# Optimization experiments

Hardware: AMD Instinct MI355X
Metric: run time of the kernel (lower is better)

The kernel has to match this reference:

```python
import jax, jax.numpy as jnp
import numpy as np

# Dims chosen per init_kwargs / input_specs
B, CIN, H, W = 16, 384, 64, 64
HEADS, HD = 4, 24
D = HEADS * HD                 # 96, per-pixel feature dim after head split
NMOD = 2                       # PartitionalClustering (hard), FuzzyClustering (soft)
NSTREAM = 1 + 2 * NMOD         # p + (k,v) per clustering module = 5
AG = 8                         # agents_hw = (8,8) -> 64 agent tokens
CL = 2                         # clusters_hw = (2,2) -> 4 clusters per module
M_PER = CL * CL
M_ALL = NMOD * M_PER           # 8 total clusters (sim_alpha/sim_beta size)


def setup_inputs() -> dict:
    key = jax.random.key(0)
    ks = jax.random.split(key, 4)
    x = jax.random.normal(ks[0], (B, CIN, H, W), jnp.float32)
    # proj: 1x1 pointwise linear CIN -> NSTREAM*D
    W1 = jax.random.normal(ks[1], (CIN, NSTREAM * D), jnp.float32) * 0.02
    b1 = jnp.zeros((NSTREAM * D,), jnp.float32)
    # proj2: 1x1 pointwise linear D -> CIN
    W2 = jax.random.normal(ks[2], (D, CIN), jnp.float32) * 0.02
    b2 = jnp.zeros((CIN,), jnp.float32)
    sim_alpha = jnp.ones((M_ALL,), jnp.float32)
    sim_beta = jnp.zeros((M_ALL,), jnp.float32)
    return {"x": x, "W1": W1, "b1": b1, "W2": W2, "b2": b2,
            "sim_alpha": sim_alpha, "sim_beta": sim_beta}


def _pool(t, oh, ow):
    # exact adaptive avg pool when h%oh==0 and w%ow==0
    b, c, h, w = t.shape
    return t.reshape(b, c, oh, h // oh, ow, w // ow).mean(axis=(3, 5))


def _cluster_agg(k, kc, v, vc, hard):
    # k: (b,c,N)  kc: (b,m,c)  v: (b,N,c)  vc: (b,m,c)
    # similarity = negative squared euclidean distance (use_cosine=False)
    d2 = (kc ** 2).sum(-1)[..., None] + (k ** 2).sum(1)[:, None, :] \
         - 2.0 * jnp.einsum('bmc,bcn->bmn', kc, k)          # (b,m,N)
    sim = -d2
    if hard:   # PartitionalClustering: hard one-hot assignment over clusters
        w = jax.nn.one_hot(jnp.argmax(sim, axis=1), sim.shape[1], axis=1, dtype=k.dtype)
    else:      # FuzzyClustering: soft assignment over clusters
        w = jax.nn.softmax(sim, axis=1)
    agg = vc + jnp.einsum('bmn,bnc->bmc', w, v)
    return agg / (1.0 + w.sum(-1, keepdims=True))            # cluster-bias normalization


def _cosine(a, p):
    # a: (b,M,c), p: (b,c,N) -> cosine similarity (b,M,N)
    an = a / (jnp.linalg.norm(a, axis=-1, keepdims=True) + 1e-6)
    pn = p / (jnp.linalg.norm(p, axis=1, keepdims=True) + 1e-6)
    return jnp.einsum('bmc,bcn->bmn', an, pn)


def reference(x, W1, b1, W2, b2, sim_alpha, sim_beta):
    # proj (1x1): (B,CIN,H,W) -> (B, NSTREAM*D, H, W)
    y = jnp.einsum('bchw,cd->bdhw', x, W1) + b1[None, :, None, None]
    b = B * HEADS
    y = y.reshape(B, NSTREAM, D, H, W).transpose(1, 0, 2, 3, 4)
    y = y.reshape(NSTREAM, b, HD, H, W)
    p = y[0]                                   # (b, HD, H, W)
    r = y[1:].reshape(NMOD, 2, b, HD, H, W)    # (module, k/v, b, HD, H, W)

    aggs = []
    for i in range(NMOD):
        k, v = r[i, 0], r[i, 1]
        kc = _pool(k, CL, CL).reshape(b, HD, M_PER).transpose(0, 2, 1)  # (b,m,c)
        vc = _pool(v, CL, CL).reshape(b, HD, M_PER).transpose(0, 2, 1)
        ka = _pool(k, AG, AG).reshape(b, HD, AG * AG)                   # (b,c,N)
        va = _pool(v, AG, AG).reshape(b, HD, AG * AG).transpose(0, 2, 1)
        aggs.append(_cluster_agg(ka, kc, va, vc, hard=(i == 0)))
    agg = jnp.concatenate(aggs, axis=1)        # (b, M_ALL, HD)

    pa = _pool(p, AG, AG).reshape(b, HD, AG * AG)                       # (b,c,N)
    sim = sim_alpha[None, :, None] * _cosine(agg, pa) + sim_beta[None, :, None]
    assign = jax.nn.softmax(sim, axis=1)        # over clusters
    out = jnp.einsum('bmc,bmn->bcn', agg, assign).reshape(b, HD, AG, AG)
    out = jax.image.resize(out, (b, HD, H, W), method='bilinear')
    out = out.reshape(B, D, H, W)
    # proj2 (1x1): D -> CIN
    return jnp.einsum('bchw,co->bohw', out, W2) + b2[None, :, None, None]
```

## Files before the change

### kernel.cpp

```cpp
#include <hip/hip_runtime.h>
#include <math.h>

#define NB     16
#define NCIN   384
#define NHD    24
#define NDIM   96
#define NSTR   5
#define NDT    480

__global__ void __launch_bounds__(256) k_pool(const float* __restrict__ x,
                                              float* __restrict__ x8) {
    __shared__ float part[64][17];
    const int plane = blockIdx.x;
    const int t = threadIdx.x;
    const float4* xp = reinterpret_cast<const float4*>(x + (size_t)plane * 4096);
    const int chunk = t & 15;
    const int rloc  = t >> 4;
#pragma unroll
    for (int rr = 0; rr < 4; ++rr) {
        int row = rr * 16 + rloc;
        float4 v = xp[rr * 256 + t];
        part[row][chunk] = v.x + v.y + v.z + v.w;
    }
    __syncthreads();
    if (t < 64) {
        int py = t >> 3, px = t & 7;
        float s = 0.f;
#pragma unroll
        for (int r = 0; r < 8; ++r)
            s += part[py * 8 + r][px * 2] + part[py * 8 + r][px * 2 + 1];
        x8[(size_t)plane * 64 + t] = s * (1.f / 64.f);
    }
}

#define KC 64
__global__ void __launch_bounds__(256) k_proj(const float* __restrict__ x8,
                                              const float* __restrict__ W1,
                                              const float* __restrict__ b1,
                                              float* __restrict__ y8) {
    __shared__ float AL[KC][32];
    __shared__ float BL[KC][64];
    const int b    = blockIdx.y >> 1;
    const int pix0 = (blockIdx.y & 1) * 32;
    const int d0   = blockIdx.x * 64;
    const int tid  = threadIdx.x;
    const int pxg  = (tid & 15) * 2;
    const int dg   = (tid >> 4) * 4;
    float acc[2][4] = {};
    for (int c0 = 0; c0 < 384; c0 += KC) {
        __syncthreads();
#pragma unroll
        for (int i = 0; i < 2; ++i) {
            int f = tid + i * 256;
            int c = f >> 3, pg = f & 7;
            *reinterpret_cast<float4*>(&AL[c][pg * 4]) =
                *reinterpret_cast<const float4*>(&x8[(b * 384 + c0 + c) * 64 + pix0 + pg * 4]);
        }
#pragma unroll
        for (int i = 0; i < 4; ++i) {
            int f = tid + i * 256;
            int c = f >> 4, jg = f & 15;
            int d = d0 + jg * 4;
            float4 v = make_float4(0.f, 0.f, 0.f, 0.f);
            if (d < NDT) v = *reinterpret_cast<const float4*>(&W1[(c0 + c) * NDT + d]);
            *reinterpret_cast<float4*>(&BL[c][jg * 4]) = v;
        }
        __syncthreads();
#pragma unroll 8
        for (int c = 0; c < KC; ++c) {
            float2 a = *reinterpret_cast<const float2*>(&AL[c][pxg]);
            float4 w = *reinterpret_cast<const float4*>(&BL[c][dg]);
            acc[0][0] += a.x * w.x; acc[0][1] += a.x * w.y;
            acc[0][2] += a.x * w.z; acc[0][3] += a.x * w.w;
            acc[1][0] += a.y * w.x; acc[1][1] += a.y * w.y;
            acc[1][2] += a.y * w.z; acc[1][3] += a.y * w.w;
        }
    }
    if (d0 + dg < NDT) {
        float4 bv = *reinterpret_cast<const float4*>(&b1[d0 + dg]);
#pragma unroll
        for (int p = 0; p < 2; ++p) {
            int pix = pix0 + pxg + p;
            float4 v = make_float4(acc[p][0] + bv.x, acc[p][1] + bv.y,
                                   acc[p][2] + bv.z, acc[p][3] + bv.w);
            *reinterpret_cast<float4*>(&y8[(size_t)(b * 64 + pix) * NDT + d0 + dg]) = v;
        }
    }
}

__global__ void __launch_bounds__(256) k_cluster(const float* __restrict__ y8,
                                                 const float* __restrict__ salpha,
                                                 const float* __restrict__ sbeta,
                                                 float* __restrict__ out8) {
    __shared__ float sl[5][64][25];
    __shared__ float y2s[5][4][24];
    __shared__ float wb[2][64][5];
    __shared__ float aggL[8][25];
    __shared__ float anL[8][24];
    __shared__ float normL[8];

    const int bp = blockIdx.x;
    const int Bi = bp >> 2, h = bp & 3;
    const int tid = threadIdx.x;
    const int lane = tid & 63, wid = tid >> 6;

    for (int idx = tid; idx < 5 * 64 * 6; idx += 256) {
        int q = idx % 6;
        int row = idx / 6;
        int pix = row & 63, s = row >> 6;
        float4 v = *reinterpret_cast<const float4*>(
            &y8[(size_t)(Bi * 64 + pix) * NDT + s * NDIM + h * NHD + q * 4]);
        int c = q * 4;
        sl[s][pix][c]     = v.x;
        sl[s][pix][c + 1] = v.y;
        sl[s][pix][c + 2] = v.z;
        sl[s][pix][c + 3] = v.w;
    }
    __syncthreads();
    for (int idx = tid; idx < 5 * 4 * 24; idx += 256) {
        int c = idx % 24;
        int m = (idx / 24) & 3;
        int s = idx / 96;
        int my = m >> 1, mx = m & 1;
        float acc = 0.f;
#pragma unroll
        for (int ry = 0; ry < 4; ++ry)
#pragma unroll
            for (int rx = 0; rx < 4; ++rx)
                acc += sl[s][(my * 4 + ry) * 8 + mx * 4 + rx][c];
        y2s[s][m][c] = acc * (1.f / 16.f);
    }
    __syncthreads();
    if (wid < 2) {
        const int i = wid, ks = 1 + 2 * i;
        float ka[24];
        float sumk2 = 0.f;
#pragma unroll
        for (int c = 0; c < 24; ++c) { ka[c] = sl[ks][lane][c]; sumk2 += ka[c] * ka[c]; }
        float sim[4];
#pragma unroll
        for (int m = 0; m < 4; ++m) {
            float kc2 = 0.f, dt = 0.f;
#pragma unroll
            for (int c = 0; c < 24; ++c) {
                float kv = y2s[ks][m][c];
                kc2 += kv * kv; dt += kv * ka[c];
            }
            sim[m] = 2.f * dt - kc2 - sumk2;
        }
        float w[4];
        if (i == 0) {
            int am = 0; float bv = sim[0];
#pragma unroll
            for (int m = 1; m < 4; ++m) if (sim[m] > bv) { bv = sim[m]; am = m; }
#pragma unroll
            for (int m = 0; m < 4; ++m) w[m] = (m == am) ? 1.f : 0.f;
        } else {
            float mx = fmaxf(fmaxf(sim[0], sim[1]), fmaxf(sim[2], sim[3]));
            float sum = 0.f;
#pragma unroll
            for (int m = 0; m < 4; ++m) { w[m] = expf(sim[m] - mx); sum += w[m]; }
            float inv = 1.f / sum;
#pragma unroll
            for (int m = 0; m < 4; ++m) w[m] *= inv;
        }
#pragma unroll
        for (int m = 0; m < 4; ++m) wb[i][lane][m] = w[m];
    }
    __syncthreads();
    if (tid < 200) {
        int i = tid / 100, rem = tid % 100;
        int m = rem / 25, c = rem % 25;
        int vs = 2 + 2 * i;
        float s = 0.f;
#pragma unroll 8
        for (int n = 0; n < 64; ++n) {
            float wv = wb[i][n][m];
            s += (c < 24) ? wv * sl[vs][n][c] : wv;
        }
        aggL[i * 4 + m][c] = s;
    }
    __syncthreads();
    if (tid < 192) {
        int mm = tid / 24, c = tid % 24;
        int i = mm >> 2, m = mm & 3;
        aggL[mm][c] = (y2s[2 + 2 * i][m][c] + aggL[mm][c]) / (1.f + aggL[mm][24]);
    }
    __syncthreads();
    if (tid < 8) {
        float s = 0.f;
#pragma unroll
        for (int c = 0; c < 24; ++c) s += aggL[tid][c] * aggL[tid][c];
        normL[tid] = sqrtf(s) + 1e-6f;
    }
    __syncthreads();
    if (tid < 192) {
        int mm = tid / 24, c = tid % 24;
        anL[mm][c] = aggL[mm][c] / normL[mm];
    }
    __syncthreads();
    {
        const int n = lane;
        float pa[24]; float p2 = 0.f;
#pragma unroll
        for (int c = 0; c < 24; ++c) { pa[c] = sl[0][n][c]; p2 += pa[c] * pa[c]; }
        float pinv = 1.f / (sqrtf(p2) + 1e-6f);
        float s2[8];
#pragma unroll
        for (int mm = 0; mm < 8; ++mm) {
            float dt = 0.f;
#pragma unroll
            for (int c = 0; c < 24; ++c) dt += anL[mm][c] * pa[c];
            s2[mm] = salpha[mm] * (dt * pinv) + sbeta[mm];
        }
        float mx = s2[0];
#pragma unroll
        for (int mm = 1; mm < 8; ++mm) mx = fmaxf(mx, s2[mm]);
        float sum = 0.f;
#pragma unroll
        for (int mm = 0; mm < 8; ++mm) { s2[mm] = expf(s2[mm] - mx); sum += s2[mm]; }
        float inv = 1.f / sum;
        const int c0 = wid * 6;
#pragma unroll
        for (int cc = 0; cc < 6; ++cc) {
            int c = c0 + cc;
            float v = 0.f;
#pragma unroll
            for (int mm = 0; mm < 8; ++mm) v += aggL[mm][c] * (s2[mm] * inv);
            out8[(size_t)(Bi * NDIM + h * NHD + c) * 64 + n] = v;
        }
    }
}

__global__ void __launch_bounds__(256) k_proj2up(const float* __restrict__ out8,
                                                 const float* __restrict__ W2,
                                                 const float* __restrict__ b2,
                                                 float* __restrict__ out) {
    __shared__ float AL[96][64];
    __shared__ float WL[96][24];
    __shared__ float ZT[24][65];
    const int Bi = blockIdx.y;
    const int o0 = blockIdx.x * 24;
    const int tid = threadIdx.x;

#pragma unroll
    for (int i = 0; i < 6; ++i) {
        int f = tid + i * 256;
        int d = f >> 4, ng = f & 15;
        *reinterpret_cast<float4*>(&AL[d][ng * 4]) =
            *reinterpret_cast<const float4*>(&out8[(size_t)(Bi * NDIM + d) * 64 + ng * 4]);
    }
    for (int idx = tid; idx < 96 * 6; idx += 256) {
        int d = idx / 6, q = idx % 6;
        *reinterpret_cast<float4*>(&WL[d][q * 4]) =
            *reinterpret_cast<const float4*>(&W2[d * NCIN + o0 + q * 4]);
    }
    __syncthreads();
    {
        const int n = tid & 63, og = tid >> 6;
        float a0 = 0.f, a1 = 0.f, a2 = 0.f, a3 = 0.f, a4 = 0.f, a5 = 0.f;
#pragma unroll 8
        for (int d = 0; d < 96; ++d) {
            float a = AL[d][n];
            float2 w01 = *reinterpret_cast<const float2*>(&WL[d][og * 6 + 0]);
            float2 w23 = *reinterpret_cast<const float2*>(&WL[d][og * 6 + 2]);
            float2 w45 = *reinterpret_cast<const float2*>(&WL[d][og * 6 + 4]);
            a0 += a * w01.x; a1 += a * w01.y;
            a2 += a * w23.x; a3 += a * w23.y;
            a4 += a * w45.x; a5 += a * w45.y;
        }
        ZT[og * 6 + 0][n] = a0;
        ZT[og * 6 + 1][n] = a1;
        ZT[og * 6 + 2][n] = a2;
        ZT[og * 6 + 3][n] = a3;
        ZT[og * 6 + 4][n] = a4;
        ZT[og * 6 + 5][n] = a5;
    }
    __syncthreads();
#pragma unroll
    for (int pass = 0; pass < 2; ++pass) {
        int slot = pass * 256 + tid;
        if (slot < 24 * 16) {
            const int ol = slot >> 4, xq = slot & 15;
            const float bias = b2[o0 + ol];

            float uxb = 0.125f * (float)(xq * 4) - 0.4375f;
            float uxbc = fminf(fmaxf(uxb, 0.f), 7.f);
            const int ixb = (int)uxbc;
            float wa[4], wbx[4], wc[4];
#pragma unroll
            for (int j = 0; j < 4; ++j) {
                float ux  = 0.125f * (float)(xq * 4 + j) - 0.4375f;
                float uxc = fminf(fmaxf(ux, 0.f), 7.f);
                int ix0 = (int)uxc;
                int ix1 = ix0 + 1 > 7 ? 7 : ix0 + 1;
                float fx = uxc - (float)ix0;
                int k0 = ix0 - ixb, k1 = ix1 - ixb;
                wa[j]  = ((k0 == 0) ? (1.f - fx) : 0.f) + ((k1 == 0) ? fx : 0.f);
                wbx[j] = ((k0 == 1) ? (1.f - fx) : 0.f) + ((k1 == 1) ? fx : 0.f);
                wc[j]  = ((k1 == 2) ? fx : 0.f);
            }
            float zc0[8], zc1[8], zc2[8];
            {
                const int i1 = ixb + 1 > 7 ? 7 : ixb + 1;
                const int i2 = ixb + 2 > 7 ? 7 : ixb + 2;
#pragma unroll
                for (int iy = 0; iy < 8; ++iy) {
                    zc0[iy] = ZT[ol][iy * 8 + ixb];
                    zc1[iy] = ZT[ol][iy * 8 + i1];
                    zc2[iy] = ZT[ol][iy * 8 + i2];
                }
            }
            float* obase = out + (size_t)(Bi * NCIN + o0 + ol) * 4096 + xq * 4;
#pragma unroll
            for (int y = 0; y < 64; ++y) {
                const float u  = 0.125f * (float)y - 0.4375f;
                const float uc = fminf(fmaxf(u, 0.f), 7.f);
                const int iy0 = (int)uc;
                const int iy1 = iy0 + 1 > 7 ? 7 : iy0 + 1;
                const float fy = uc - (float)iy0;
                const float r0 = zc0[iy0] + fy * (zc0[iy1] - zc0[iy0]);
                const float r1 = zc1[iy0] + fy * (zc1[iy1] - zc1[iy0]);
                const float r2 = zc2[iy0] + fy * (zc2[iy1] - zc2[iy0]);
                float4 v;
                v.x = bias + wa[0] * r0 + wbx[0] * r1 + wc[0] * r2;
                v.y = bias + wa[1] * r0 + wbx[1] * r1 + wc[1] * r2;
                v.z = bias + wa[2] * r0 + wbx[2] * r1 + wc[2] * r2;
                v.w = bias + wa[3] * r0 + wbx[3] * r1 + wc[3] * r2;
                *reinterpret_cast<float4*>(obase + y * 64) = v;
            }
        }
    }
}

extern "C" void kernel_launch(void* const* d_in, const int* in_sizes, int n_in,
                              void* d_out, int out_size, void* d_ws, size_t ws_size,
                              hipStream_t stream) {
    const float* x  = (const float*)d_in[0];
    const float* W1 = (const float*)d_in[1];
    const float* b1 = (const float*)d_in[2];
    const float* W2 = (const float*)d_in[3];
    const float* b2 = (const float*)d_in[4];
    const float* sa = (const float*)d_in[5];
    const float* sb = (const float*)d_in[6];
    float* out = (float*)d_out;

    float* x8 = (float*)d_ws;
    float* y8 = x8 + 16 * 384 * 64;
    float* o8 = y8 + 1024 * 480;

    k_pool<<<dim3(16 * 384), dim3(256), 0, stream>>>(x, x8);
    k_proj<<<dim3(8, 32), dim3(256), 0, stream>>>(x8, W1, b1, y8);
    k_cluster<<<dim3(64), dim3(256), 0, stream>>>(y8, sa, sb, o8);
    k_proj2up<<<dim3(16, 16), dim3(256), 0, stream>>>(o8, W2, b2, out);
}
```

Measured before the change: 68.30 us.

## Fuse pool, projection, clustering and upsample into one cooperative kernel

Replaces the four separate kernel launches with a single cooperative kernel of 256 blocks, 16 per batch image. Stages are separated by per-batch atomic counter barriers in global memory, and shared memory is reused across stages through one flat buffer. The aim is to remove launch gaps between stages. In exchange, the pooling stage loses most of its parallelism: each block now walks 24 planes one after another with a block sync per plane, instead of spreading the work over thousands of blocks. Most blocks also sit idle during the clustering stage.

```diff
diff --git a/kernel.cpp b/kernel.cpp
--- a/kernel.cpp
+++ b/kernel.cpp
@@ -8,328 +8,359 @@
 #define NSTR   5
 #define NDT    480
 
-__global__ void __launch_bounds__(256) k_pool(const float* __restrict__ x,
-                                              float* __restrict__ x8) {
-    __shared__ float part[64][17];
-    const int plane = blockIdx.x;
-    const int t = threadIdx.x;
-    const float4* xp = reinterpret_cast<const float4*>(x + (size_t)plane * 4096);
-    const int chunk = t & 15;
-    const int rloc  = t >> 4;
-#pragma unroll
-    for (int rr = 0; rr < 4; ++rr) {
-        int row = rr * 16 + rloc;
-        float4 v = xp[rr * 256 + t];
-        part[row][chunk] = v.x + v.y + v.z + v.w;
-    }
+
+__device__ __forceinline__ void group_barrier(int* c, int target) {
+    __threadfence();
     __syncthreads();
-    if (t < 64) {
-        int py = t >> 3, px = t & 7;
-        float s = 0.f;
-#pragma unroll
-        for (int r = 0; r < 8; ++r)
-            s += part[py * 8 + r][px * 2] + part[py * 8 + r][px * 2 + 1];
-        x8[(size_t)plane * 64 + t] = s * (1.f / 64.f);
-    }
+    if (threadIdx.x == 0) {
+        __hip_atomic_fetch_add(c, 1, __ATOMIC_RELEASE, __HIP_MEMORY_SCOPE_AGENT);
+        while (__hip_atomic_load(c, __ATOMIC_ACQUIRE, __HIP_MEMORY_SCOPE_AGENT) < target)
+            __builtin_amdgcn_s_sleep(2);
+    }
+    __syncthreads();
+    __threadfence();
 }
 
-#define KC 64
-__global__ void __launch_bounds__(256) k_proj(const float* __restrict__ x8,
-                                              const float* __restrict__ W1,
-                                              const float* __restrict__ b1,
-                                              float* __restrict__ y8) {
-    __shared__ float AL[KC][32];
-    __shared__ float BL[KC][64];
-    const int b    = blockIdx.y >> 1;
-    const int pix0 = (blockIdx.y & 1) * 32;
-    const int d0   = blockIdx.x * 64;
-    const int tid  = threadIdx.x;
-    const int pxg  = (tid & 15) * 2;
-    const int dg   = (tid >> 4) * 4;
-    float acc[2][4] = {};
-    for (int c0 = 0; c0 < 384; c0 += KC) {
-        __syncthreads();
-#pragma unroll
-        for (int i = 0; i < 2; ++i) {
+__global__ void __launch_bounds__(256) k_fused(const float* __restrict__ x,
+                                               const float* __restrict__ W1,
+                                               const float* __restrict__ b1,
+                                               const float* __restrict__ W2,
+                                               const float* __restrict__ b2,
+                                               const float* __restrict__ salpha,
+                                               const float* __restrict__ sbeta,
+                                               float* __restrict__ out,
+                                               float* __restrict__ x8,
+                                               float* __restrict__ y8,
+                                               float* __restrict__ o8,
+                                               int* __restrict__ flags) {
+    __shared__ __align__(16) float smem[10100];
+    const int g   = blockIdx.x;
+    const int b   = g >> 4;
+    const int sub = g & 15;
+    const int tid = threadIdx.x;
+    int* cnt = flags + b * 3;
+
+    {
+        #define PART(r,cc) smem[(r)*17+(cc)]
+        const int chunk = tid & 15;
+        const int rloc  = tid >> 4;
+        for (int i = 0; i < 24; ++i) {
+            const int c = sub * 24 + i;
+            const float4* xp = reinterpret_cast<const float4*>(x + ((size_t)(b * 384 + c)) * 4096);
+#pragma unroll
+            for (int rr = 0; rr < 4; ++rr) {
+                int row = rr * 16 + rloc;
+                float4 v = xp[rr * 256 + tid];
+                PART(row, chunk) = v.x + v.y + v.z + v.w;
+            }
+            __syncthreads();
+            if (tid < 64) {
+                int py = tid >> 3, px = tid & 7;
+                float s = 0.f;
+#pragma unroll
+                for (int r = 0; r < 8; ++r)
+                    s += PART(py * 8 + r, px * 2) + PART(py * 8 + r, px * 2 + 1);
+                x8[(size_t)(b * 384 + c) * 64 + tid] = s * (1.f / 64.f);
+            }
+            __syncthreads();
+        }
+        #undef PART
+    }
+    group_barrier(cnt + 0, 16);
+
+    {
+        #define PAL(c,p) smem[(c)*32+(p)]
+        #define PBL(c,d) smem[2048+(c)*64+(d)]
+        const int pix0 = (sub >> 3) * 32;
+        const int d0   = (sub & 7) * 64;
+        const int pxg  = (tid & 15) * 2;
+        const int dg   = (tid >> 4) * 4;
+        float acc[2][4] = {};
+        for (int c0 = 0; c0 < 384; c0 += 64) {
+            __syncthreads();
+#pragma unroll
+            for (int i = 0; i < 2; ++i) {
+                int f = tid + i * 256;
+                int c = f >> 3, pg = f & 7;
+                *reinterpret_cast<float4*>(&PAL(c, pg * 4)) =
+                    *reinterpret_cast<const float4*>(&x8[(size_t)(b * 384 + c0 + c) * 64 + pix0 + pg * 4]);
+            }
+#pragma unroll
+            for (int i = 0; i < 4; ++i) {
+                int f = tid + i * 256;
+                int c = f >> 4, jg = f & 15;
+                int d = d0 + jg * 4;
+                float4 v = make_float4(0.f, 0.f, 0.f, 0.f);
+                if (d < NDT) v = *reinterpret_cast<const float4*>(&W1[(c0 + c) * NDT + d]);
+                *reinterpret_cast<float4*>(&PBL(c, jg * 4)) = v;
+            }
+            __syncthreads();
+#pragma unroll 8
+            for (int c = 0; c < 64; ++c) {
+                float2 a = *reinterpret_cast<const float2*>(&PAL(c, pxg));
+                float4 w = *reinterpret_cast<const float4*>(&PBL(c, dg));
+                acc[0][0] += a.x * w.x; acc[0][1] += a.x * w.y;
+                acc[0][2] += a.x * w.z; acc[0][3] += a.x * w.w;
+                acc[1][0] += a.y * w.x; acc[1][1] += a.y * w.y;
+                acc[1][2] += a.y * w.z; acc[1][3] += a.y * w.w;
+            }
+        }
+        if (d0 + dg < NDT) {
+            float4 bv = *reinterpret_cast<const float4*>(&b1[d0 + dg]);
+#pragma unroll
+            for (int p = 0; p < 2; ++p) {
+                int pix = pix0 + pxg + p;
+                float4 v = make_float4(acc[p][0] + bv.x, acc[p][1] + bv.y,
+                                       acc[p][2] + bv.z, acc[p][3] + bv.w);
+                *reinterpret_cast<float4*>(&y8[(size_t)(b * 64 + pix) * NDT + d0 + dg]) = v;
+            }
+        }
+        #undef PAL
+        #undef PBL
+    }
+    group_barrier(cnt + 1, 16);
+
+    if (sub < 4) {
+        #define SL(s,p,c)  smem[(s)*1600+(p)*25+(c)]
+        #define Y2S(s,m,c) smem[8000+((s)*4+(m))*24+(c)]
+        #define WBM(i,n,m) smem[8480+((i)*64+(n))*5+(m)]
+        #define AGG(mm,c)  smem[9120+(mm)*25+(c)]
+        #define ANL(mm,c)  smem[9320+(mm)*24+(c)]
+        #define NRM(mm)    smem[9512+(mm)]
+        const int Bi = b, h = sub;
+        const int lane = tid & 63, wid = tid >> 6;
+
+        for (int idx = tid; idx < 5 * 64 * 6; idx += 256) {
+            int q = idx % 6;
+            int row = idx / 6;
+            int pix = row & 63, s = row >> 6;
+            float4 v = *reinterpret_cast<const float4*>(
+                &y8[(size_t)(Bi * 64 + pix) * NDT + s * NDIM + h * NHD + q * 4]);
+            int c = q * 4;
+            SL(s, pix, c)     = v.x;
+            SL(s, pix, c + 1) = v.y;
+            SL(s, pix, c + 2) = v.z;
+            SL(s, pix, c + 3) = v.w;
+        }
+        __syncthreads();
+        for (int idx = tid; idx < 5 * 4 * 24; idx += 256) {
+            int c = idx % 24;
+            int m = (idx / 24) & 3;
+            int s = idx / 96;
+            int my = m >> 1, mx = m & 1;
+            float acc = 0.f;
+#pragma unroll
+            for (int ry = 0; ry < 4; ++ry)
+#pragma unroll
+                for (int rx = 0; rx < 4; ++rx)
+                    acc += SL(s, (my * 4 + ry) * 8 + mx * 4 + rx, c);
+            Y2S(s, m, c) = acc * (1.f / 16.f);
+        }
+        __syncthreads();
+        if (wid < 2) {
+            const int i = wid, ks = 1 + 2 * i;
+            float ka[24];
+            float sumk2 = 0.f;
+#pragma unroll
+            for (int c = 0; c < 24; ++c) { ka[c] = SL(ks, lane, c); sumk2 += ka[c] * ka[c]; }
+            float sim[4];
+#pragma unroll
+            for (int m = 0; m < 4; ++m) {
+                float kc2 = 0.f, dt = 0.f;
+#pragma unroll
+                for (int c = 0; c < 24; ++c) {
+                    float kv = Y2S(ks, m, c);
+                    kc2 += kv * kv; dt += kv * ka[c];
+                }
+                sim[m] = 2.f * dt - kc2 - sumk2;
+            }
+            float w[4];
+            if (i == 0) {
+                int am = 0; float bv = sim[0];
+#pragma unroll
+                for (int m = 1; m < 4; ++m) if (sim[m] > bv) { bv = sim[m]; am = m; }
+#pragma unroll
+                for (int m = 0; m < 4; ++m) w[m] = (m == am) ? 1.f : 0.f;
+            } else {
+                float mx = fmaxf(fmaxf(sim[0], sim[1]), fmaxf(sim[2], sim[3]));
+                float sum = 0.f;
+#pragma unroll
+                for (int m = 0; m < 4; ++m) { w[m] = expf(sim[m] - mx); sum += w[m]; }
+                float inv = 1.f / sum;
+#pragma unroll
+                for (int m = 0; m < 4; ++m) w[m] *= inv;
+            }
+#pragma unroll
+            for (int m = 0; m < 4; ++m) WBM(i, lane, m) = w[m];
+        }
+        __syncthreads();
+        if (tid < 200) {
+            int i = tid / 100, rem = tid % 100;
+            int m = rem / 25, c = rem % 25;
+            int vs = 2 + 2 * i;
+            float s = 0.f;
+#pragma unroll 8
+            for (int n = 0; n < 64; ++n) {
+                float wv = WBM(i, n, m);
+                s += (c < 24) ? wv * SL(vs, n, c) : wv;
+            }
+            AGG(i * 4 + m, c) = s;
+        }
+        __syncthreads();
+        if (tid < 192) {
+            int mm = tid / 24, c = tid % 24;
+            int i = mm >> 2, m = mm & 3;
+            AGG(mm, c) = (Y2S(2 + 2 * i, m, c) + AGG(mm, c)) / (1.f + AGG(mm, 24));
+        }
+        __syncthreads();
+        if (tid < 8) {
+            float s = 0.f;
+#pragma unroll
+            for (int c = 0; c < 24; ++c) s += AGG(tid, c) * AGG(tid, c);
+            NRM(tid) = sqrtf(s) + 1e-6f;
+        }
+        __syncthreads();
+        if (tid < 192) {
+            int mm = tid / 24, c = tid % 24;
+            ANL(mm, c) = AGG(mm, c) / NRM(mm);
+        }
+        __syncthreads();
+        {
+            const int n = lane;
+            float pa[24]; float p2 = 0.f;
+#pragma unroll
+            for (int c = 0; c < 24; ++c) { pa[c] = SL(0, n, c); p2 += pa[c] * pa[c]; }
+            float pinv = 1.f / (sqrtf(p2) + 1e-6f);
+            float s2[8];
+#pragma unroll
+            for (int mm = 0; mm < 8; ++mm) {
+                float dt = 0.f;
+#pragma unroll
+                for (int c = 0; c < 24; ++c) dt += ANL(mm, c) * pa[c];
+                s2[mm] = salpha[mm] * (dt * pinv) + sbeta[mm];
+            }
+            float mx = s2[0];
+#pragma unroll
+            for (int mm = 1; mm < 8; ++mm) mx = fmaxf(mx, s2[mm]);
+            float sum = 0.f;
+#pragma unroll
+            for (int mm = 0; mm < 8; ++mm) { s2[mm] = expf(s2[mm] - mx); sum += s2[mm]; }
+            float inv = 1.f / sum;
+            const int c0 = wid * 6;
+#pragma unroll
+            for (int cc = 0; cc < 6; ++cc) {
+                int c = c0 + cc;
+                float v = 0.f;
+#pragma unroll
+                for (int mm = 0; mm < 8; ++mm) v += AGG(mm, c) * (s2[mm] * inv);
+                o8[(size_t)(Bi * NDIM + h * NHD + c) * 64 + n] = v;
+            }
+        }
+        #undef SL
+        #undef Y2S
+        #undef WBM
+        #undef AGG
+        #undef ANL
+        #undef NRM
+    }
+    group_barrier(cnt + 2, 16);
+
+    {
+        #define DAL(d,n) smem[(d)*64+(n)]
+        #define DWL(d,o) smem[6144+(d)*24+(o)]
+        #define DZT(o,n) smem[8448+(o)*65+(n)]
+        const int o0 = sub * 24;
+#pragma unroll
+        for (int i = 0; i < 6; ++i) {
             int f = tid + i * 256;
-            int c = f >> 3, pg = f & 7;
-            *reinterpret_cast<float4*>(&AL[c][pg * 4]) =
-                *reinterpret_cast<const float4*>(&x8[(b * 384 + c0 + c) * 64 + pix0 + pg * 4]);
-        }
-#pragma unroll
-        for (int i = 0; i < 4; ++i) {
-            int f = tid + i * 256;
-            int c = f >> 4, jg = f & 15;
-            int d = d0 + jg * 4;
-            float4 v = make_float4(0.f, 0.f, 0.f, 0.f);
-            if (d < NDT) v = *reinterpret_cast<const float4*>(&W1[(c0 + c) * NDT + d]);
-            *reinterpret_cast<float4*>(&BL[c][jg * 4]) = v;
-        }
-        __syncthreads();
+            int d = f >> 4, ng = f & 15;
+            *reinterpret_cast<float4*>(&DAL(d, ng * 4)) =
+                *reinterpret_cast<const float4*>(&o8[(size_t)(b * NDIM + d) * 64 + ng * 4]);
+        }
+        for (int idx = tid; idx < 96 * 6; idx += 256) {
+            int d = idx / 6, q = idx % 6;
+            *reinterpret_cast<float4*>(&DWL(d, q * 4)) =
+                *reinterpret_cast<const float4*>(&W2[d * NCIN + o0 + q * 4]);
+        }
+        __syncthreads();
+        {
+            const int n = tid & 63, og = tid >> 6;
+            float a0 = 0.f, a1 = 0.f, a2 = 0.f, a3 = 0.f, a4 = 0.f, a5 = 0.f;
 #pragma unroll 8
-        for (int c = 0; c < KC; ++c) {
-            float2 a = *reinterpret_cast<const float2*>(&AL[c][pxg]);
-            float4 w = *reinterpret_cast<const float4*>(&BL[c][dg]);
-            acc[0][0] += a.x * w.x; acc[0][1] += a.x * w.y;
-            acc[0][2] += a.x * w.z; acc[0][3] += a.x * w.w;
-            acc[1][0] += a.y * w.x; acc[1][1] += a.y * w.y;
-            acc[1][2] += a.y * w.z; acc[1][3] += a.y * w.w;
-        }
-    }
-    if (d0 + dg < NDT) {
-        float4 bv = *reinterpret_cast<const float4*>(&b1[d0 + dg]);
-#pragma unroll
-        for (int p = 0; p < 2; ++p) {
-            int pix = pix0 + pxg + p;
-            float4 v = make_float4(acc[p][0] + bv.x, acc[p][1] + bv.y,
-                                   acc[p][2] + bv.z, acc[p][3] + bv.w);
-            *reinterpret_cast<float4*>(&y8[(size_t)(b * 64 + pix) * NDT + d0 + dg]) = v;
-        }
-    }
-}
-
-__global__ void __launch_bounds__(256) k_cluster(const float* __restrict__ y8,
-                                                 const float* __restrict__ salpha,
-                                                 const float* __restrict__ sbeta,
-                                                 float* __restrict__ out8) {
-    __shared__ float sl[5][64][25];
-    __shared__ float y2s[5][4][24];
-    __shared__ float wb[2][64][5];
-    __shared__ float aggL[8][25];
-    __shared__ float anL[8][24];
-    __shared__ float normL[8];
-
-    const int bp = blockIdx.x;
-    const int Bi = bp >> 2, h = bp & 3;
-    const int tid = threadIdx.x;
-    const int lane = tid & 63, wid = tid >> 6;
-
-    for (int idx = tid; idx < 5 * 64 * 6; idx += 256) {
-        int q = idx % 6;
-        int row = idx / 6;
-        int pix = row & 63, s = row >> 6;
-        float4 v = *reinterpret_cast<const float4*>(
-            &y8[(size_t)(Bi * 64 + pix) * NDT + s * NDIM + h * NHD + q * 4]);
-        int c = q * 4;
-        sl[s][pix][c]     = v.x;
-        sl[s][pix][c + 1] = v.y;
-        sl[s][pix][c + 2] = v.z;
-        sl[s][pix][c + 3] = v.w;
-    }
-    __syncthreads();
-    for (int idx = tid; idx < 5 * 4 * 24; idx += 256) {
-        int c = idx % 24;
-        int m = (idx / 24) & 3;
-        int s = idx / 96;
-        int my = m >> 1, mx = m & 1;
-        float acc = 0.f;
-#pragma unroll
-        for (int ry = 0; ry < 4; ++ry)
-#pragma unroll
-            for (int rx = 0; rx < 4; ++rx)
-                acc += sl[s][(my * 4 + ry) * 8 + mx * 4 + rx][c];
-        y2s[s][m][c] = acc * (1.f / 16.f);
-    }
-    __syncthreads();
-    if (wid < 2) {
-        const int i = wid, ks = 1 + 2 * i;
-        float ka[24];
-        float sumk2 = 0.f;
-#pragma unroll
-        for (int c = 0; c < 24; ++c) { ka[c] = sl[ks][lane][c]; sumk2 += ka[c] * ka[c]; }
-        float sim[4];
-#pragma unroll
-        for (int m = 0; m < 4; ++m) {
-            float kc2 = 0.f, dt = 0.f;
-#pragma unroll
-            for (int c = 0; c < 24; ++c) {
-                float kv = y2s[ks][m][c];
-                kc2 += kv * kv; dt += kv * ka[c];
-            }
-            sim[m] = 2.f * dt - kc2 - sumk2;
-        }
-        float w[4];
-        if (i == 0) {
-            int am = 0; float bv = sim[0];
-#pragma unroll
-            for (int m = 1; m < 4; ++m) if (sim[m] > bv) { bv = sim[m]; am = m; }
-#pragma unroll
-            for (int m = 0; m < 4; ++m) w[m] = (m == am) ? 1.f : 0.f;
-        } else {
-            float mx = fmaxf(fmaxf(sim[0], sim[1]), fmaxf(sim[2], sim[3]));
-            float sum = 0.f;
-#pragma unroll
-            for (int m = 0; m < 4; ++m) { w[m] = expf(sim[m] - mx); sum += w[m]; }
-            float inv = 1.f / sum;
-#pragma unroll
-            for (int m = 0; m < 4; ++m) w[m] *= inv;
-        }
-#pragma unroll
-        for (int m = 0; m < 4; ++m) wb[i][lane][m] = w[m];
-    }
-    __syncthreads();
-    if (tid < 200) {
-        int i = tid / 100, rem = tid % 100;
-        int m = rem / 25, c = rem % 25;
-        int vs = 2 + 2 * i;
-        float s = 0.f;
-#pragma unroll 8
-        for (int n = 0; n < 64; ++n) {
-            float wv = wb[i][n][m];
-            s += (c < 24) ? wv * sl[vs][n][c] : wv;
-        }
-        aggL[i * 4 + m][c] = s;
-    }
-    __syncthreads();
-    if (tid < 192) {
-        int mm = tid / 24, c = tid % 24;
-        int i = mm >> 2, m = mm & 3;
-        aggL[mm][c] = (y2s[2 + 2 * i][m][c] + aggL[mm][c]) / (1.f + aggL[mm][24]);
-    }
-    __syncthreads();
-    if (tid < 8) {
-        float s = 0.f;
-#pragma unroll
-        for (int c = 0; c < 24; ++c) s += aggL[tid][c] * aggL[tid][c];
-        normL[tid] = sqrtf(s) + 1e-6f;
-    }
-    __syncthreads();
-    if (tid < 192) {
-        int mm = tid / 24, c = tid % 24;
-        anL[mm][c] = aggL[mm][c] / normL[mm];
-    }
-    __syncthreads();
-    {
-        const int n = lane;
-        float pa[24]; float p2 = 0.f;
-#pragma unroll
-        for (int c = 0; c < 24; ++c) { pa[c] = sl[0][n][c]; p2 += pa[c] * pa[c]; }
-        float pinv = 1.f / (sqrtf(p2) + 1e-6f);
-        float s2[8];
-#pragma unroll
-        for (int mm = 0; mm < 8; ++mm) {
-            float dt = 0.f;
-#pragma unroll
-            for (int c = 0; c < 24; ++c) dt += anL[mm][c] * pa[c];
-            s2[mm] = salpha[mm] * (dt * pinv) + sbeta[mm];
-        }
-        float mx = s2[0];
-#pragma unroll
-        for (int mm = 1; mm < 8; ++mm) mx = fmaxf(mx, s2[mm]);
-        float sum = 0.f;
-#pragma unroll
-        for (int mm = 0; mm < 8; ++mm) { s2[mm] = expf(s2[mm] - mx); sum += s2[mm]; }
-        float inv = 1.f / sum;
-        const int c0 = wid * 6;
-#pragma unroll
-        for (int cc = 0; cc < 6; ++cc) {
-            int c = c0 + cc;
-            float v = 0.f;
-#pragma unroll
-            for (int mm = 0; mm < 8; ++mm) v += aggL[mm][c] * (s2[mm] * inv);
-            out8[(size_t)(Bi * NDIM + h * NHD + c) * 64 + n] = v;
-        }
-    }
-}
-
-__global__ void __launch_bounds__(256) k_proj2up(const float* __restrict__ out8,
-                                                 const float* __restrict__ W2,
-                                                 const float* __restrict__ b2,
-                                                 float* __restrict__ out) {
-    __shared__ float AL[96][64];
-    __shared__ float WL[96][24];
-    __shared__ float ZT[24][65];
-    const int Bi = blockIdx.y;
-    const int o0 = blockIdx.x * 24;
-    const int tid = threadIdx.x;
-
-#pragma unroll
-    for (int i = 0; i < 6; ++i) {
-        int f = tid + i * 256;
-        int d = f >> 4, ng = f & 15;
-        *reinterpret_cast<float4*>(&AL[d][ng * 4]) =
-            *reinterpret_cast<const float4*>(&out8[(size_t)(Bi * NDIM + d) * 64 + ng * 4]);
-    }
-    for (int idx = tid; idx < 96 * 6; idx += 256) {
-        int d = idx / 6, q = idx % 6;
-        *reinterpret_cast<float4*>(&WL[d][q * 4]) =
-            *reinterpret_cast<const float4*>(&W2[d * NCIN + o0 + q * 4]);
-    }
-    __syncthreads();
-    {
-        const int n = tid & 63, og = tid >> 6;
-        float a0 = 0.f, a1 = 0.f, a2 = 0.f, a3 = 0.f, a4 = 0.f, a5 = 0.f;
-#pragma unroll 8
-        for (int d = 0; d < 96; ++d) {
-            float a = AL[d][n];
-            float2 w01 = *reinterpret_cast<const float2*>(&WL[d][og * 6 + 0]);
-            float2 w23 = *reinterpret_cast<const float2*>(&WL[d][og * 6 + 2]);
-            float2 w45 = *reinterpret_cast<const float2*>(&WL[d][og * 6 + 4]);
-            a0 += a * w01.x; a1 += a * w01.y;
-            a2 += a * w23.x; a3 += a * w23.y;
-            a4 += a * w45.x; a5 += a * w45.y;
-        }
-        ZT[og * 6 + 0][n] = a0;
-        ZT[og * 6 + 1][n] = a1;
-        ZT[og * 6 + 2][n] = a2;
-        ZT[og * 6 + 3][n] = a3;
-        ZT[og * 6 + 4][n] = a4;
-        ZT[og * 6 + 5][n] = a5;
-    }
-    __syncthreads();
-#pragma unroll
-    for (int pass = 0; pass < 2; ++pass) {
-        int slot = pass * 256 + tid;
-        if (slot < 24 * 16) {
-            const int ol = slot >> 4, xq = slot & 15;
-            const float bias = b2[o0 + ol];
-
-            float uxb = 0.125f * (float)(xq * 4) - 0.4375f;
-            float uxbc = fminf(fmaxf(uxb, 0.f), 7.f);
-            const int ixb = (int)uxbc;
-            float wa[4], wbx[4], wc[4];
-#pragma unroll
-            for (int j = 0; j < 4; ++j) {
-                float ux  = 0.125f * (float)(xq * 4 + j) - 0.4375f;
-                float uxc = fminf(fmaxf(ux, 0.f), 7.f);
-                int ix0 = (int)uxc;
-                int ix1 = ix0 + 1 > 7 ? 7 : ix0 + 1;
-                float fx = uxc - (float)ix0;
-                int k0 = ix0 - ixb, k1 = ix1 - ixb;
-                wa[j]  = ((k0 == 0) ? (1.f - fx) : 0.f) + ((k1 == 0) ? fx : 0.f);
-                wbx[j] = ((k0 == 1) ? (1.f - fx) : 0.f) + ((k1 == 1) ? fx : 0.f);
-                wc[j]  = ((k1 == 2) ? fx : 0.f);
-            }
-            float zc0[8], zc1[8], zc2[8];
-            {
-                const int i1 = ixb + 1 > 7 ? 7 : ixb + 1;
-                const int i2 = ixb + 2 > 7 ? 7 : ixb + 2;
-#pragma unroll
-                for (int iy = 0; iy < 8; ++iy) {
-                    zc0[iy] = ZT[ol][iy * 8 + ixb];
-                    zc1[iy] = ZT[ol][iy * 8 + i1];
-                    zc2[iy] = ZT[ol][iy * 8 + i2];
+            for (int d = 0; d < 96; ++d) {
+                float a = DAL(d, n);
+                float2 w01 = *reinterpret_cast<const float2*>(&DWL(d, og * 6 + 0));
+                float2 w23 = *reinterpret_cast<const float2*>(&DWL(d, og * 6 + 2));
+                float2 w45 = *reinterpret_cast<const float2*>(&DWL(d, og * 6 + 4));
+                a0 += a * w01.x; a1 += a * w01.y;
+                a2 += a * w23.x; a3 += a * w23.y;
+                a4 += a * w45.x; a5 += a * w45.y;
+            }
+            DZT(og * 6 + 0, n) = a0;
+            DZT(og * 6 + 1, n) = a1;
+            DZT(og * 6 + 2, n) = a2;
+            DZT(og * 6 + 3, n) = a3;
+            DZT(og * 6 + 4, n) = a4;
+            DZT(og * 6 + 5, n) = a5;
+        }
+        __syncthreads();
+#pragma unroll
+        for (int pass = 0; pass < 2; ++pass) {
+            int slot = pass * 256 + tid;
+            if (slot < 24 * 16) {
+                const int ol = slot >> 4, xq = slot & 15;
+                const float bias = b2[o0 + ol];
+
+                float uxb = 0.125f * (float)(xq * 4) - 0.4375f;
+                float uxbc = fminf(fmaxf(uxb, 0.f), 7.f);
+                const int ixb = (int)uxbc;
+                float wa[4], wbx[4], wc[4];
+#pragma unroll
+                for (int j = 0; j < 4; ++j) {
+                    float ux  = 0.125f * (float)(xq * 4 + j) - 0.4375f;
+                    float uxc = fminf(fmaxf(ux, 0.f), 7.f);
+                    int ix0 = (int)uxc;
+                    int ix1 = ix0 + 1 > 7 ? 7 : ix0 + 1;
+                    float fx = uxc - (float)ix0;
+                    int k0 = ix0 - ixb, k1 = ix1 - ixb;
+                    wa[j]  = ((k0 == 0) ? (1.f - fx) : 0.f) + ((k1 == 0) ? fx : 0.f);
+                    wbx[j] = ((k0 == 1) ? (1.f - fx) : 0.f) + ((k1 == 1) ? fx : 0.f);
+                    wc[j]  = ((k1 == 2) ? fx : 0.f);
                 }
-            }
-            float* obase = out + (size_t)(Bi * NCIN + o0 + ol) * 4096 + xq * 4;
-#pragma unroll
-            for (int y = 0; y < 64; ++y) {
-                const float u  = 0.125f * (float)y - 0.4375f;
-                const float uc = fminf(fmaxf(u, 0.f), 7.f);
-                const int iy0 = (int)uc;
-                const int iy1 = iy0 + 1 > 7 ? 7 : iy0 + 1;
-                const float fy = uc - (float)iy0;
-                const float r0 = zc0[iy0] + fy * (zc0[iy1] - zc0[iy0]);
-                const float r1 = zc1[iy0] + fy * (zc1[iy1] - zc1[iy0]);
-                const float r2 = zc2[iy0] + fy * (zc2[iy1] - zc2[iy0]);
-                float4 v;
-                v.x = bias + wa[0] * r0 + wbx[0] * r1 + wc[0] * r2;
-                v.y = bias + wa[1] * r0 + wbx[1] * r1 + wc[1] * r2;
-                v.z = bias + wa[2] * r0 + wbx[2] * r1 + wc[2] * r2;
-                v.w = bias + wa[3] * r0 + wbx[3] * r1 + wc[3] * r2;
-                *reinterpret_cast<float4*>(obase + y * 64) = v;
-            }
-        }
+                float zc0[8], zc1[8], zc2[8];
+                {
+                    const int i1 = ixb + 1 > 7 ? 7 : ixb + 1;
+                    const int i2 = ixb + 2 > 7 ? 7 : ixb + 2;
+#pragma unroll
+                    for (int iy = 0; iy < 8; ++iy) {
+                        zc0[iy] = DZT(ol, iy * 8 + ixb);
+                        zc1[iy] = DZT(ol, iy * 8 + i1);
+                        zc2[iy] = DZT(ol, iy * 8 + i2);
+                    }
+                }
+                float* obase = out + (size_t)(b * NCIN + o0 + ol) * 4096 + xq * 4;
+#pragma unroll
+                for (int y = 0; y < 64; ++y) {
+                    const float u  = 0.125f * (float)y - 0.4375f;
+                    const float uc = fminf(fmaxf(u, 0.f), 7.f);
+                    const int iy0 = (int)uc;
+                    const int iy1 = iy0 + 1 > 7 ? 7 : iy0 + 1;
+                    const float fy = uc - (float)iy0;
+                    const float r0 = zc0[iy0] + fy * (zc0[iy1] - zc0[iy0]);
+                    const float r1 = zc1[iy0] + fy * (zc1[iy1] - zc1[iy0]);
+                    const float r2 = zc2[iy0] + fy * (zc2[iy1] - zc2[iy0]);
+                    float4 v;
+                    v.x = bias + wa[0] * r0 + wbx[0] * r1 + wc[0] * r2;
+                    v.y = bias + wa[1] * r0 + wbx[1] * r1 + wc[1] * r2;
+                    v.z = bias + wa[2] * r0 + wbx[2] * r1 + wc[2] * r2;
+                    v.w = bias + wa[3] * r0 + wbx[3] * r1 + wc[3] * r2;
+                    *reinterpret_cast<float4*>(obase + y * 64) = v;
+                }
+            }
+        }
+        #undef DAL
+        #undef DWL
+        #undef DZT
     }
 }
 
@@ -348,9 +379,13 @@
     float* x8 = (float*)d_ws;
     float* y8 = x8 + 16 * 384 * 64;
     float* o8 = y8 + 1024 * 480;
-
-    k_pool<<<dim3(16 * 384), dim3(256), 0, stream>>>(x, x8);
-    k_proj<<<dim3(8, 32), dim3(256), 0, stream>>>(x8, W1, b1, y8);
-    k_cluster<<<dim3(64), dim3(256), 0, stream>>>(y8, sa, sb, o8);
-    k_proj2up<<<dim3(16, 16), dim3(256), 0, stream>>>(o8, W2, b2, out);
+    int* flags = (int*)(o8 + 16 * 96 * 64);
+
+    hipMemsetAsync(flags, 0, 64 * sizeof(int), stream);
+
+    void* args[] = {(void*)&x, (void*)&W1, (void*)&b1, (void*)&W2, (void*)&b2,
+                    (void*)&sa, (void*)&sb, (void*)&out, (void*)&x8, (void*)&y8,
+                    (void*)&o8, (void*)&flags};
+    hipLaunchCooperativeKernel((const void*)k_fused, dim3(256), dim3(256),
+                               args, 0, stream);
 }
```

Result: slower. 235.2 us (+244.3%).

## Fuse cluster aggregation into proj2+upsample kernel with low-rank projection

Applied to the files above, without the earlier changes.

Merges the clustering kernel into the final projection/upsample kernel. Each of the 256 blocks redundantly recomputes the cluster aggregation for all four heads of its batch and stores the agents and assignments in shared memory. The 96-dim proj2 is then refactored as (agg·W2) followed by assignment weighting over 32 cluster rows, so the intermediate out8 buffer and one launch disappear. The trade is 16x redundant cluster work per batch and serial per-head loops in exchange for removing a launch and a global round trip.

```diff
diff --git a/kernel.cpp b/kernel.cpp
--- a/kernel.cpp
+++ b/kernel.cpp
@@ -33,13 +33,12 @@
     }
 }
 
-#define KC 64
 __global__ void __launch_bounds__(256) k_proj(const float* __restrict__ x8,
                                               const float* __restrict__ W1,
                                               const float* __restrict__ b1,
                                               float* __restrict__ y8) {
-    __shared__ float AL[KC][32];
-    __shared__ float BL[KC][64];
+    __shared__ float AL[64][32];
+    __shared__ float BL[64][64];
     const int b    = blockIdx.y >> 1;
     const int pix0 = (blockIdx.y & 1) * 32;
     const int d0   = blockIdx.x * 64;
@@ -47,7 +46,7 @@
     const int pxg  = (tid & 15) * 2;
     const int dg   = (tid >> 4) * 4;
     float acc[2][4] = {};
-    for (int c0 = 0; c0 < 384; c0 += KC) {
+    for (int c0 = 0; c0 < 384; c0 += 64) {
         __syncthreads();
 #pragma unroll
         for (int i = 0; i < 2; ++i) {
@@ -67,7 +66,7 @@
         }
         __syncthreads();
 #pragma unroll 8
-        for (int c = 0; c < KC; ++c) {
+        for (int c = 0; c < 64; ++c) {
             float2 a = *reinterpret_cast<const float2*>(&AL[c][pxg]);
             float4 w = *reinterpret_cast<const float4*>(&BL[c][dg]);
             acc[0][0] += a.x * w.x; acc[0][1] += a.x * w.y;
@@ -88,195 +87,202 @@
     }
 }
 
-__global__ void __launch_bounds__(256) k_cluster(const float* __restrict__ y8,
-                                                 const float* __restrict__ salpha,
-                                                 const float* __restrict__ sbeta,
-                                                 float* __restrict__ out8) {
-    __shared__ float sl[5][64][25];
-    __shared__ float y2s[5][4][24];
-    __shared__ float wb[2][64][5];
-    __shared__ float aggL[8][25];
-    __shared__ float anL[8][24];
-    __shared__ float normL[8];
-
-    const int bp = blockIdx.x;
-    const int Bi = bp >> 2, h = bp & 3;
+__global__ void __launch_bounds__(256) k_cpu(const float* __restrict__ y8,
+                                             const float* __restrict__ W2,
+                                             const float* __restrict__ b2,
+                                             const float* __restrict__ salpha,
+                                             const float* __restrict__ sbeta,
+                                             float* __restrict__ out) {
+    __shared__ __align__(16) float smem[12968];
+    #define SL(sp,p,c)  smem[(sp)*1600+(p)*25+(c)]
+    #define Y2S(sp,m,c) smem[6400+((sp)*4+(m))*24+(c)]
+    #define WBM(i,n,m)  smem[6784+((i)*64+(n))*5+(m)]
+    #define AGG(mm,c)   smem[7424+(mm)*25+(c)]
+    #define NRM(mm)     smem[7624+(mm)]
+    #define ANL(mm,c)   smem[7632+(mm)*24+(c)]
+    #define AGA(k,c)    smem[7824+(k)*24+(c)]
+    #define ASG(k,n)    smem[8592+(k)*64+(n)]
+    #define GM(k,o)     smem[10640+(k)*24+(o)]
+    #define ZT(o,n)     smem[11408+(o)*65+(n)]
+    #define W2L(d,o)    smem[(d)*24+(o)]
+
+    const int b  = blockIdx.y;
+    const int o0 = blockIdx.x * 24;
     const int tid = threadIdx.x;
     const int lane = tid & 63, wid = tid >> 6;
 
-    for (int idx = tid; idx < 5 * 64 * 6; idx += 256) {
-        int q = idx % 6;
-        int row = idx / 6;
-        int pix = row & 63, s = row >> 6;
-        float4 v = *reinterpret_cast<const float4*>(
-            &y8[(size_t)(Bi * 64 + pix) * NDT + s * NDIM + h * NHD + q * 4]);
-        int c = q * 4;
-        sl[s][pix][c]     = v.x;
-        sl[s][pix][c + 1] = v.y;
-        sl[s][pix][c + 2] = v.z;
-        sl[s][pix][c + 3] = v.w;
-    }
-    __syncthreads();
-    for (int idx = tid; idx < 5 * 4 * 24; idx += 256) {
-        int c = idx % 24;
-        int m = (idx / 24) & 3;
-        int s = idx / 96;
-        int my = m >> 1, mx = m & 1;
-        float acc = 0.f;
-#pragma unroll
-        for (int ry = 0; ry < 4; ++ry)
-#pragma unroll
-            for (int rx = 0; rx < 4; ++rx)
-                acc += sl[s][(my * 4 + ry) * 8 + mx * 4 + rx][c];
-        y2s[s][m][c] = acc * (1.f / 16.f);
-    }
-    __syncthreads();
-    if (wid < 2) {
-        const int i = wid, ks = 1 + 2 * i;
-        float ka[24];
-        float sumk2 = 0.f;
-#pragma unroll
-        for (int c = 0; c < 24; ++c) { ka[c] = sl[ks][lane][c]; sumk2 += ka[c] * ka[c]; }
-        float sim[4];
-#pragma unroll
-        for (int m = 0; m < 4; ++m) {
-            float kc2 = 0.f, dt = 0.f;
-#pragma unroll
-            for (int c = 0; c < 24; ++c) {
-                float kv = y2s[ks][m][c];
-                kc2 += kv * kv; dt += kv * ka[c];
-            }
-            sim[m] = 2.f * dt - kc2 - sumk2;
-        }
-        float w[4];
-        if (i == 0) {
-            int am = 0; float bv = sim[0];
-#pragma unroll
-            for (int m = 1; m < 4; ++m) if (sim[m] > bv) { bv = sim[m]; am = m; }
-#pragma unroll
-            for (int m = 0; m < 4; ++m) w[m] = (m == am) ? 1.f : 0.f;
-        } else {
-            float mx = fmaxf(fmaxf(sim[0], sim[1]), fmaxf(sim[2], sim[3]));
+    for (int h = 0; h < 4; ++h) {
+        if (h) __syncthreads();
+        for (int idx = tid; idx < 4 * 64 * 6; idx += 256) {
+            int q = idx % 6;
+            int row = idx / 6;
+            int pix = row & 63, sp = row >> 6;
+            float4 v = *reinterpret_cast<const float4*>(
+                &y8[(size_t)(b * 64 + pix) * NDT + (sp + 1) * NDIM + h * NHD + q * 4]);
+            int c = q * 4;
+            SL(sp, pix, c)     = v.x;
+            SL(sp, pix, c + 1) = v.y;
+            SL(sp, pix, c + 2) = v.z;
+            SL(sp, pix, c + 3) = v.w;
+        }
+        __syncthreads();
+        for (int idx = tid; idx < 4 * 4 * 24; idx += 256) {
+            int c = idx % 24;
+            int m = (idx / 24) & 3;
+            int sp = idx / 96;
+            int my = m >> 1, mx = m & 1;
+            float acc = 0.f;
+#pragma unroll
+            for (int ry = 0; ry < 4; ++ry)
+#pragma unroll
+                for (int rx = 0; rx < 4; ++rx)
+                    acc += SL(sp, (my * 4 + ry) * 8 + mx * 4 + rx, c);
+            Y2S(sp, m, c) = acc * (1.f / 16.f);
+        }
+        __syncthreads();
+        if (wid < 2) {
+            const int i = wid, ksp = 2 * i;
+            float ka[24];
+            float sumk2 = 0.f;
+#pragma unroll
+            for (int c = 0; c < 24; ++c) { ka[c] = SL(ksp, lane, c); sumk2 += ka[c] * ka[c]; }
+            float sim[4];
+#pragma unroll
+            for (int m = 0; m < 4; ++m) {
+                float kc2 = 0.f, dt = 0.f;
+#pragma unroll
+                for (int c = 0; c < 24; ++c) {
+                    float kv = Y2S(ksp, m, c);
+                    kc2 += kv * kv; dt += kv * ka[c];
+                }
+                sim[m] = 2.f * dt - kc2 - sumk2;
+            }
+            float w[4];
+            if (i == 0) {
+                int am = 0; float bv = sim[0];
+#pragma unroll
+                for (int m = 1; m < 4; ++m) if (sim[m] > bv) { bv = sim[m]; am = m; }
+#pragma unroll
+                for (int m = 0; m < 4; ++m) w[m] = (m == am) ? 1.f : 0.f;
+            } else {
+                float mx = fmaxf(fmaxf(sim[0], sim[1]), fmaxf(sim[2], sim[3]));
+                float sum = 0.f;
+#pragma unroll
+                for (int m = 0; m < 4; ++m) { w[m] = expf(sim[m] - mx); sum += w[m]; }
+                float inv = 1.f / sum;
+#pragma unroll
+                for (int m = 0; m < 4; ++m) w[m] *= inv;
+            }
+#pragma unroll
+            for (int m = 0; m < 4; ++m) WBM(i, lane, m) = w[m];
+        }
+        __syncthreads();
+        if (tid < 200) {
+            int i = tid / 100, rem = tid % 100;
+            int m = rem / 25, c = rem % 25;
+            int vsp = 1 + 2 * i;
+            float s = 0.f;
+#pragma unroll 8
+            for (int n = 0; n < 64; ++n) {
+                float wv = WBM(i, n, m);
+                s += (c < 24) ? wv * SL(vsp, n, c) : wv;
+            }
+            AGG(i * 4 + m, c) = s;
+        }
+        __syncthreads();
+        if (tid < 192) {
+            int mm = tid / 24, c = tid % 24;
+            int i = mm >> 2, m = mm & 3;
+            AGA(h * 8 + mm, c) = (Y2S(1 + 2 * i, m, c) + AGG(mm, c)) / (1.f + AGG(mm, 24));
+        }
+        __syncthreads();
+        if (tid < 8) {
+            float s = 0.f;
+#pragma unroll
+            for (int c = 0; c < 24; ++c) s += AGA(h * 8 + tid, c) * AGA(h * 8 + tid, c);
+            NRM(tid) = sqrtf(s) + 1e-6f;
+        }
+        __syncthreads();
+        if (tid < 192) {
+            int mm = tid / 24, c = tid % 24;
+            ANL(mm, c) = AGA(h * 8 + mm, c) / NRM(mm);
+        }
+        __syncthreads();
+        if (wid == 0) {
+            const int n = lane;
+            float pa[24]; float p2 = 0.f;
+            const float* prow = &y8[(size_t)(b * 64 + n) * NDT + h * NHD];
+#pragma unroll
+            for (int q = 0; q < 6; ++q) {
+                float4 v = *reinterpret_cast<const float4*>(prow + q * 4);
+                pa[q * 4 + 0] = v.x; pa[q * 4 + 1] = v.y;
+                pa[q * 4 + 2] = v.z; pa[q * 4 + 3] = v.w;
+            }
+#pragma unroll
+            for (int c = 0; c < 24; ++c) p2 += pa[c] * pa[c];
+            float pinv = 1.f / (sqrtf(p2) + 1e-6f);
+            float s2[8];
+#pragma unroll
+            for (int mm = 0; mm < 8; ++mm) {
+                float dt = 0.f;
+#pragma unroll
+                for (int c = 0; c < 24; ++c) dt += ANL(mm, c) * pa[c];
+                s2[mm] = salpha[mm] * (dt * pinv) + sbeta[mm];
+            }
+            float mx = s2[0];
+#pragma unroll
+            for (int mm = 1; mm < 8; ++mm) mx = fmaxf(mx, s2[mm]);
             float sum = 0.f;
 #pragma unroll
-            for (int m = 0; m < 4; ++m) { w[m] = expf(sim[m] - mx); sum += w[m]; }
+            for (int mm = 0; mm < 8; ++mm) { s2[mm] = expf(s2[mm] - mx); sum += s2[mm]; }
             float inv = 1.f / sum;
 #pragma unroll
-            for (int m = 0; m < 4; ++m) w[m] *= inv;
-        }
-#pragma unroll
-        for (int m = 0; m < 4; ++m) wb[i][lane][m] = w[m];
-    }
-    __syncthreads();
-    if (tid < 200) {
-        int i = tid / 100, rem = tid % 100;
-        int m = rem / 25, c = rem % 25;
-        int vs = 2 + 2 * i;
-        float s = 0.f;
-#pragma unroll 8
-        for (int n = 0; n < 64; ++n) {
-            float wv = wb[i][n][m];
-            s += (c < 24) ? wv * sl[vs][n][c] : wv;
-        }
-        aggL[i * 4 + m][c] = s;
-    }
-    __syncthreads();
-    if (tid < 192) {
-        int mm = tid / 24, c = tid % 24;
-        int i = mm >> 2, m = mm & 3;
-        aggL[mm][c] = (y2s[2 + 2 * i][m][c] + aggL[mm][c]) / (1.f + aggL[mm][24]);
-    }
-    __syncthreads();
-    if (tid < 8) {
-        float s = 0.f;
-#pragma unroll
-        for (int c = 0; c < 24; ++c) s += aggL[tid][c] * aggL[tid][c];
-        normL[tid] = sqrtf(s) + 1e-6f;
-    }
-    __syncthreads();
-    if (tid < 192) {
-        int mm = tid / 24, c = tid % 24;
-        anL[mm][c] = aggL[mm][c] / normL[mm];
-    }
-    __syncthreads();
-    {
-        const int n = lane;
-        float pa[24]; float p2 = 0.f;
-#pragma unroll
-        for (int c = 0; c < 24; ++c) { pa[c] = sl[0][n][c]; p2 += pa[c] * pa[c]; }
-        float pinv = 1.f / (sqrtf(p2) + 1e-6f);
-        float s2[8];
-#pragma unroll
-        for (int mm = 0; mm < 8; ++mm) {
-            float dt = 0.f;
-#pragma unroll
-            for (int c = 0; c < 24; ++c) dt += anL[mm][c] * pa[c];
-            s2[mm] = salpha[mm] * (dt * pinv) + sbeta[mm];
-        }
-        float mx = s2[0];
-#pragma unroll
-        for (int mm = 1; mm < 8; ++mm) mx = fmaxf(mx, s2[mm]);
-        float sum = 0.f;
-#pragma unroll
-        for (int mm = 0; mm < 8; ++mm) { s2[mm] = expf(s2[mm] - mx); sum += s2[mm]; }
-        float inv = 1.f / sum;
-        const int c0 = wid * 6;
-#pragma unroll
-        for (int cc = 0; cc < 6; ++cc) {
-            int c = c0 + cc;
-            float v = 0.f;
-#pragma unroll
-            for (int mm = 0; mm < 8; ++mm) v += aggL[mm][c] * (s2[mm] * inv);
-            out8[(size_t)(Bi * NDIM + h * NHD + c) * 64 + n] = v;
-        }
-    }
-}
-
-__global__ void __launch_bounds__(256) k_proj2up(const float* __restrict__ out8,
-                                                 const float* __restrict__ W2,
-                                                 const float* __restrict__ b2,
-                                                 float* __restrict__ out) {
-    __shared__ float AL[96][64];
-    __shared__ float WL[96][24];
-    __shared__ float ZT[24][65];
-    const int Bi = blockIdx.y;
-    const int o0 = blockIdx.x * 24;
-    const int tid = threadIdx.x;
-
-#pragma unroll
-    for (int i = 0; i < 6; ++i) {
-        int f = tid + i * 256;
-        int d = f >> 4, ng = f & 15;
-        *reinterpret_cast<float4*>(&AL[d][ng * 4]) =
-            *reinterpret_cast<const float4*>(&out8[(size_t)(Bi * NDIM + d) * 64 + ng * 4]);
-    }
+            for (int mm = 0; mm < 8; ++mm)
+                ASG(h * 8 + mm, n) = s2[mm] * inv;
+        }
+    }
+    __syncthreads();
+
     for (int idx = tid; idx < 96 * 6; idx += 256) {
         int d = idx / 6, q = idx % 6;
-        *reinterpret_cast<float4*>(&WL[d][q * 4]) =
-            *reinterpret_cast<const float4*>(&W2[d * NCIN + o0 + q * 4]);
-    }
-    __syncthreads();
-    {
-        const int n = tid & 63, og = tid >> 6;
-        float a0 = 0.f, a1 = 0.f, a2 = 0.f, a3 = 0.f, a4 = 0.f, a5 = 0.f;
-#pragma unroll 8
-        for (int d = 0; d < 96; ++d) {
-            float a = AL[d][n];
-            float2 w01 = *reinterpret_cast<const float2*>(&WL[d][og * 6 + 0]);
-            float2 w23 = *reinterpret_cast<const float2*>(&WL[d][og * 6 + 2]);
-            float2 w45 = *reinterpret_cast<const float2*>(&WL[d][og * 6 + 4]);
-            a0 += a * w01.x; a1 += a * w01.y;
-            a2 += a * w23.x; a3 += a * w23.y;
-            a4 += a * w45.x; a5 += a * w45.y;
-        }
-        ZT[og * 6 + 0][n] = a0;
-        ZT[og * 6 + 1][n] = a1;
-        ZT[og * 6 + 2][n] = a2;
-        ZT[og * 6 + 3][n] = a3;
-        ZT[og * 6 + 4][n] = a4;
-        ZT[og * 6 + 5][n] = a5;
-    }
-    __syncthreads();
+        float4 v = *reinterpret_cast<const float4*>(&W2[d * NCIN + o0 + q * 4]);
+        W2L(d, q * 4 + 0) = v.x; W2L(d, q * 4 + 1) = v.y;
+        W2L(d, q * 4 + 2) = v.z; W2L(d, q * 4 + 3) = v.w;
+    }
+    __syncthreads();
+#pragma unroll
+    for (int r = 0; r < 3; ++r) {
+        int idx = tid + r * 256;
+        int k = idx / 24, o = idx % 24;
+        int dbase = (k >> 3) * 24;
+        float s = 0.f;
+#pragma unroll
+        for (int c = 0; c < 24; ++c)
+            s += AGA(k, c) * W2L(dbase + c, o);
+        GM(k, o) = s;
+    }
+    __syncthreads();
+
+#pragma unroll
+    for (int r = 0; r < 2; ++r) {
+        int idx = tid + r * 256;
+        if (idx < 24 * 16) {
+            int o = idx >> 4, ng = idx & 15;
+            float z0 = 0.f, z1 = 0.f, z2 = 0.f, z3 = 0.f;
+#pragma unroll
+            for (int k = 0; k < 32; ++k) {
+                float g = GM(k, o);
+                float4 a = *reinterpret_cast<const float4*>(&ASG(k, ng * 4));
+                z0 += g * a.x; z1 += g * a.y; z2 += g * a.z; z3 += g * a.w;
+            }
+            ZT(o, ng * 4 + 0) = z0;
+            ZT(o, ng * 4 + 1) = z1;
+            ZT(o, ng * 4 + 2) = z2;
+            ZT(o, ng * 4 + 3) = z3;
+        }
+    }
+    __syncthreads();
+
 #pragma unroll
     for (int pass = 0; pass < 2; ++pass) {
         int slot = pass * 256 + tid;
@@ -306,12 +312,12 @@
                 const int i2 = ixb + 2 > 7 ? 7 : ixb + 2;
 #pragma unroll
                 for (int iy = 0; iy < 8; ++iy) {
-                    zc0[iy] = ZT[ol][iy * 8 + ixb];
-                    zc1[iy] = ZT[ol][iy * 8 + i1];
-                    zc2[iy] = ZT[ol][iy * 8 + i2];
+                    zc0[iy] = ZT(ol, iy * 8 + ixb);
+                    zc1[iy] = ZT(ol, iy * 8 + i1);
+                    zc2[iy] = ZT(ol, iy * 8 + i2);
                 }
             }
-            float* obase = out + (size_t)(Bi * NCIN + o0 + ol) * 4096 + xq * 4;
+            float* obase = out + (size_t)(b * NCIN + o0 + ol) * 4096 + xq * 4;
 #pragma unroll
             for (int y = 0; y < 64; ++y) {
                 const float u  = 0.125f * (float)y - 0.4375f;
@@ -331,6 +337,17 @@
             }
         }
     }
+    #undef SL
+    #undef Y2S
+    #undef WBM
+    #undef AGG
+    #undef NRM
+    #undef ANL
+    #undef AGA
+    #undef ASG
+    #undef GM
+    #undef ZT
+    #undef W2L
 }
 
 extern "C" void kernel_launch(void* const* d_in, const int* in_sizes, int n_in,
@@ -347,10 +364,8 @@
 
     float* x8 = (float*)d_ws;
     float* y8 = x8 + 16 * 384 * 64;
-    float* o8 = y8 + 1024 * 480;
 
     k_pool<<<dim3(16 * 384), dim3(256), 0, stream>>>(x, x8);
     k_proj<<<dim3(8, 32), dim3(256), 0, stream>>>(x8, W1, b1, y8);
-    k_cluster<<<dim3(64), dim3(256), 0, stream>>>(y8, sa, sb, o8);
-    k_proj2up<<<dim3(16, 16), dim3(256), 0, stream>>>(o8, W2, b2, out);
+    k_cpu<<<dim3(16, 16), dim3(256), 0, stream>>>(y8, W2, b2, sa, sb, out);
 }
```

After: 87.06 us. +27.5%, slower.
